# Kernel optimization log

Hardware: AMD Instinct MI355X
Metric: run time of the kernel (lower is better)

The kernel has to match this reference:

```python
import jax, jax.numpy as jnp
from jax import lax
import numpy as np

RANK, OUT_C, IN_C, K = 4, 128, 128, 3
B, H, W = 32, 56, 56


def setup_inputs() -> dict:
    key = jax.random.key(0)
    ks = jax.random.split(key, 7)
    x = jax.random.normal(ks[0], (B, IN_C, H, W), dtype=jnp.float32)
    # init_weights_normal per rank -> plain gaussian with fan-in scaling
    w = jax.random.normal(ks[1], (RANK, OUT_C, IN_C, K, K), dtype=jnp.float32) / np.sqrt(IN_C * K * K)
    cw_row = jax.random.normal(ks[2], (RANK, H, 1), dtype=jnp.float32) * 0.1
    cw_col = jax.random.normal(ks[3], (RANK, 1, W), dtype=jnp.float32) * 0.1
    b_row = jax.random.normal(ks[4], (1, 1, H, 1), dtype=jnp.float32) * 0.01
    b_col = jax.random.normal(ks[5], (1, 1, 1, W), dtype=jnp.float32) * 0.01
    b = jax.random.normal(ks[6], (1, OUT_C, 1, 1), dtype=jnp.float32) * 0.01
    return {"x": x, "w": w, "cw_row": cw_row, "cw_col": cw_col,
            "b_row": b_row, "b_col": b_col, "b": b}


def reference(x, w, cw_row, cw_col, b_row, b_col, b):
    # lrlc_nan branch: one big conv with rank*out_channels filters,
    # then per-spatial-location low-rank combining weights.
    rank, oc, ic, kh, kw = w.shape
    w_flat = w.reshape(rank * oc, ic, kh, kw)
    convs = lax.conv_general_dilated(
        x, w_flat,
        window_strides=(1, 1),
        padding=((1, 1), (1, 1)),
        dimension_numbers=("NCHW", "OIHW", "NCHW"),
    )  # [B, rank*oc, H, W]
    bsz = x.shape[0]
    hh, ww = convs.shape[2], convs.shape[3]
    convs = convs.reshape(bsz, rank, oc, hh, ww)
    # softmax over rank of per-location combining weights [rank, H, W]
    cw = jax.nn.softmax(cw_row + cw_col, axis=0)
    out = jnp.einsum("bkcxy,kxy->bcxy", convs, cw)
    # bias_pd: per-channel + per-row + per-col biases
    out = out + b + b_col + b_row
    return out
```

## Files before the change

### kernel.cpp

```cpp
#include <hip/hip_runtime.h>

#define NB 32
#define NC 128
#define NH 56
#define NW 56
#define HP 58
#define WP 58
#define KK 1152
#define NPOS 3136
#define XT_BYTES (NB * HP * WP * NC * 2)
#define AW_OFF XT_BYTES

typedef __attribute__((ext_vector_type(8))) short s16x8;
typedef __attribute__((ext_vector_type(4))) float f32x4;
typedef unsigned int u32;

__device__ __forceinline__ unsigned short f2bf(float f) {
    union { float f; unsigned int u; } v; v.f = f;
    unsigned int u = v.u + 0x7fffu + ((v.u >> 16) & 1u);
    return (unsigned short)(u >> 16);
}

__device__ __forceinline__ void gld16(const void* g, void* l) {
    __builtin_amdgcn_global_load_lds(
        (const __attribute__((address_space(1))) u32*)g,
        (__attribute__((address_space(3))) u32*)l, 16, 0, 0);
}

__global__ void k_pro(const float* __restrict__ x, const float* __restrict__ w,
                      unsigned short* __restrict__ xt, unsigned short* __restrict__ aw) {
    int blk = blockIdx.x;
    int tid = threadIdx.x;
    if (blk >= 1792) {
        int idx = (blk - 1792) * 256 + tid;
        if (idx < 512 * KK) {
            int j = idx & 7, lane = (idx >> 3) & 63, mt = (idx >> 9) & 31, s = idx >> 14;
            int m = mt * 16 + (lane & 15);
            int kg = s * 32 + (lane >> 4) * 8 + j;
            int g = kg >> 7, ic = kg & 127;
            aw[idx] = f2bf(w[(m * 128 + ic) * 9 + g]);
        }
        return;
    }
    __shared__ unsigned short tile[128 * 57];
    int b = blk / NH, y = blk % NH;
    const float* xb = x + (size_t)b * (NC * NPOS) + y * NW;
#pragma unroll
    for (int p = 0; p < 7; ++p) {
        int idx = p * 256 + tid;
        int c = idx / 14, i = idx - c * 14;
        float4 v = *(const float4*)(xb + c * NPOS + i * 4);
        unsigned short* tp = &tile[c * 57 + i * 4];
        tp[0] = f2bf(v.x); tp[1] = f2bf(v.y); tp[2] = f2bf(v.z); tp[3] = f2bf(v.w);
    }
    __syncthreads();
    unsigned short* xrow = xt + ((size_t)(b * HP + y + 1) * WP + 1) * NC;
#pragma unroll
    for (int p = 0; p < 4; ++p) {
        int idx = p * 256 + tid;
        if (idx < 896) {
            int xp = idx >> 4, cgi = idx & 15;
            s16x8 v8;
#pragma unroll
            for (int j = 0; j < 8; ++j)
                v8[j] = (short)tile[(cgi * 8 + j) * 57 + xp];
            *(s16x8*)(xrow + xp * NC + cgi * 8) = v8;
        }
    }
    if (tid < 128) {
        xt[((size_t)(b * HP + y + 1) * WP + 0) * NC + tid] = 0;
        xt[((size_t)(b * HP + y + 1) * WP + 57) * NC + tid] = 0;
    }
    if (y == 0) {
        unsigned short* r0 = xt + (size_t)(b * HP + 0) * WP * NC;
        for (int i = tid; i < WP * NC; i += 256) r0[i] = 0;
    }
    if (y == 55) {
        unsigned short* r57 = xt + (size_t)(b * HP + 57) * WP * NC;
        for (int i = tid; i < WP * NC; i += 256) r57[i] = 0;
    }
}

__global__ void __launch_bounds__(512, 2) k_main(
    const unsigned short* __restrict__ xt, const unsigned short* __restrict__ aw,
    const float* __restrict__ cwr, const float* __restrict__ cwc,
    const float* __restrict__ brow, const float* __restrict__ bcol,
    const float* __restrict__ bch, float* __restrict__ out) {
    __shared__ __align__(16) unsigned char ldsB[2][28672];

    const int tid = threadIdx.x;
    const int lane = tid & 63;
    const int wv = tid >> 6;
    const int l15 = lane & 15, quad = lane >> 4;
    const int ph = (wv & 1) * 2;
    const int blk = blockIdx.x;
    const int b = blk / 28;
    const int tile0 = (blk - b * 28) * 112;

    const unsigned char* xt_b = (const unsigned char*)xt + (size_t)b * (HP * WP * NC * 2);
    const unsigned char* gA = (const unsigned char*)aw + wv * 1024 + lane * 16;

    const unsigned char* gB[4];
    if (wv < 7) {
#pragma unroll
        for (int h = 0; h < 4; ++h) {
            int rl = h * 4 + (lane >> 4);
            int row = wv * 16 + rl;
            int pos = tile0 + row;
            int yy = pos / 56, xx = pos - yy * 56;
            int c = (lane & 15) ^ rl;
            gB[h] = xt_b + ((yy + 1) * WP + (xx + 1)) * (NC * 2) + c * 16;
        }
    }

    s16x8 Areg[2][4];
    f32x4 acc[4][7] = {};

    auto aload = [&](int s32, int pp) {
#pragma unroll
        for (int r = 0; r < 4; ++r)
            Areg[pp][r] = *(const s16x8*)(gA + s32 * 32768 + r * 8192);
    };
    auto bissue = [&](int st, int buf) {
        if (wv < 7) {
            int dy = (st * 11) >> 5, dx = st - dy * 3;
            int off = ((dy - 1) * WP + (dx - 1)) * (NC * 2);
            unsigned char* L = &ldsB[buf][wv * 4096];
#pragma unroll
            for (int h = 0; h < 4; ++h) gld16(gB[h] + off, L + h * 1024);
        }
    };

    aload(ph, 0);
    bissue(0, 0);
    __syncthreads();

    for (int st = 0; st < 9; ++st) {
        const int cur = st & 1;
        if (st < 8) bissue(st + 1, cur ^ 1);
        const unsigned char* L = &ldsB[cur][0];
#pragma unroll
        for (int j = 0; j < 4; ++j) {
            const int kkw = (j + ph) & 3;
            if (!(st == 8 && j == 3)) {
                int nslice = (j < 3) ? st * 4 + (((j + 1) + ph) & 3)
                                     : (st + 1) * 4 + ph;
                aload(nslice, (j + 1) & 1);
            }
            s16x8 bf[7];
#pragma unroll
            for (int t = 0; t < 7; ++t)
                bf[t] = *(const s16x8*)(L + (t * 16 + l15) * 256
                                          + (((kkw * 4 + quad) ^ l15) << 4));
#pragma unroll
            for (int r = 0; r < 4; ++r)
#pragma unroll
                for (int t = 0; t < 7; ++t)
                    acc[r][t] = __builtin_amdgcn_mfma_f32_16x16x32_bf16(
                        Areg[j & 1][r], bf[t], acc[r][t], 0, 0, 0);
        }
        __syncthreads();
    }

#pragma unroll
    for (int t = 0; t < 7; ++t) {
        int pos = tile0 + t * 16 + l15;
        int yy = pos / 56, xx = pos - yy * 56;
        float v0 = cwr[yy]       + cwc[xx];
        float v1 = cwr[56 + yy]  + cwc[56 + xx];
        float v2 = cwr[112 + yy] + cwc[112 + xx];
        float v3 = cwr[168 + yy] + cwc[168 + xx];
        float mx = fmaxf(fmaxf(v0, v1), fmaxf(v2, v3));
        float e0 = __expf(v0 - mx), e1 = __expf(v1 - mx);
        float e2 = __expf(v2 - mx), e3 = __expf(v3 - mx);
        float inv = 1.0f / (e0 + e1 + e2 + e3);
        float c0 = e0 * inv, c1 = e1 * inv, c2 = e2 * inv, c3 = e3 * inv;
        float rb = brow[yy] + bcol[xx];
#pragma unroll
        for (int r = 0; r < 4; ++r) {
            int ch = wv * 16 + quad * 4 + r;
            float v = acc[0][t][r] * c0 + acc[1][t][r] * c1
                    + acc[2][t][r] * c2 + acc[3][t][r] * c3;
            out[((size_t)b * NC + ch) * NPOS + pos] = v + bch[ch] + rb;
        }
    }
}

extern "C" void kernel_launch(void* const* d_in, const int* in_sizes, int n_in,
                              void* d_out, int out_size, void* d_ws, size_t ws_size,
                              hipStream_t stream) {
    const float* x    = (const float*)d_in[0];
    const float* w    = (const float*)d_in[1];
    const float* cwr  = (const float*)d_in[2];
    const float* cwc  = (const float*)d_in[3];
    const float* brow = (const float*)d_in[4];
    const float* bcol = (const float*)d_in[5];
    const float* bch  = (const float*)d_in[6];
    float* out = (float*)d_out;

    unsigned char* ws = (unsigned char*)d_ws;
    unsigned short* xt = (unsigned short*)ws;
    unsigned short* aw = (unsigned short*)(ws + AW_OFF);

    k_pro<<<4096, 256, 0, stream>>>(x, w, xt, aw);
    k_main<<<NB * 28, 512, 0, stream>>>(xt, aw, cwr, cwc, brow, bcol, bch, out);
}
```

Measured before the change: 231.0 us.

## Rewrite prologue transpose without LDS and vectorize weight packing stores

The prologue kernel now converts x to padded NHWC bf16 with one thread per (batch, row, x, 8-channel group). Each thread does strided global loads across channels and a single 16-byte store, replacing the LDS tile transpose. Weight packing now writes 8 bf16 values per thread in one vector store, and halo zeroing moves into separate blocks that use 16-byte stores. The aim is to remove the LDS round trip and the serialized per-block padding loops, at the cost of less coalesced strided loads from x.

```diff
diff --git a/kernel.cpp b/kernel.cpp
--- a/kernel.cpp
+++ b/kernel.cpp
@@ -27,57 +27,61 @@
         (__attribute__((address_space(3))) u32*)l, 16, 0, 0);
 }
 
+#define XPB 7168
+#define WPB 7456
+#define PROGRID 7912
+
 __global__ void k_pro(const float* __restrict__ x, const float* __restrict__ w,
                       unsigned short* __restrict__ xt, unsigned short* __restrict__ aw) {
     int blk = blockIdx.x;
     int tid = threadIdx.x;
-    if (blk >= 1792) {
-        int idx = (blk - 1792) * 256 + tid;
-        if (idx < 512 * KK) {
-            int j = idx & 7, lane = (idx >> 3) & 63, mt = (idx >> 9) & 31, s = idx >> 14;
-            int m = mt * 16 + (lane & 15);
-            int kg = s * 32 + (lane >> 4) * 8 + j;
-            int g = kg >> 7, ic = kg & 127;
-            aw[idx] = f2bf(w[(m * 128 + ic) * 9 + g]);
+    if (blk < XPB) {
+        int t = blk * 256 + tid;
+        int xp = t & 63;
+        int unit = t >> 6;
+        int cgi = unit & 15;
+        int by = unit >> 4;
+        int y = by % 56, b = by / 56;
+        if (xp < 56) {
+            const float* xs = x + ((size_t)(b * 128 + cgi * 8) * NPOS) + y * 56 + xp;
+            s16x8 v;
+#pragma unroll
+            for (int j = 0; j < 8; ++j)
+                v[j] = (short)f2bf(xs[(size_t)j * NPOS]);
+            *(s16x8*)(xt + (((size_t)(b * HP + y + 1) * WP) + (xp + 1)) * NC + cgi * 8) = v;
         }
         return;
     }
-    __shared__ unsigned short tile[128 * 57];
-    int b = blk / NH, y = blk % NH;
-    const float* xb = x + (size_t)b * (NC * NPOS) + y * NW;
-#pragma unroll
-    for (int p = 0; p < 7; ++p) {
-        int idx = p * 256 + tid;
-        int c = idx / 14, i = idx - c * 14;
-        float4 v = *(const float4*)(xb + c * NPOS + i * 4);
-        unsigned short* tp = &tile[c * 57 + i * 4];
-        tp[0] = f2bf(v.x); tp[1] = f2bf(v.y); tp[2] = f2bf(v.z); tp[3] = f2bf(v.w);
-    }
-    __syncthreads();
-    unsigned short* xrow = xt + ((size_t)(b * HP + y + 1) * WP + 1) * NC;
-#pragma unroll
-    for (int p = 0; p < 4; ++p) {
-        int idx = p * 256 + tid;
-        if (idx < 896) {
-            int xp = idx >> 4, cgi = idx & 15;
-            s16x8 v8;
-#pragma unroll
-            for (int j = 0; j < 8; ++j)
-                v8[j] = (short)tile[(cgi * 8 + j) * 57 + xp];
-            *(s16x8*)(xrow + xp * NC + cgi * 8) = v8;
-        }
-    }
-    if (tid < 128) {
-        xt[((size_t)(b * HP + y + 1) * WP + 0) * NC + tid] = 0;
-        xt[((size_t)(b * HP + y + 1) * WP + 57) * NC + tid] = 0;
-    }
-    if (y == 0) {
-        unsigned short* r0 = xt + (size_t)(b * HP + 0) * WP * NC;
-        for (int i = tid; i < WP * NC; i += 256) r0[i] = 0;
-    }
-    if (y == 55) {
-        unsigned short* r57 = xt + (size_t)(b * HP + 57) * WP * NC;
-        for (int i = tid; i < WP * NC; i += 256) r57[i] = 0;
+    if (blk < WPB) {
+        int t = (blk - XPB) * 256 + tid;
+        int lane = t & 63;
+        int mt = (t >> 6) & 31;
+        int s = t >> 11;
+        int m = mt * 16 + (lane & 15);
+        int kgb = s * 32 + (lane >> 4) * 8;
+        int g = kgb >> 7, icb = kgb & 127;
+        const float* ws = w + ((size_t)m * 128 + icb) * 9 + g;
+        s16x8 v;
+#pragma unroll
+        for (int j = 0; j < 8; ++j)
+            v[j] = (short)f2bf(ws[j * 9]);
+        *(s16x8*)(aw + (size_t)t * 8) = v;
+        return;
+    }
+    int h = (blk - WPB) * 256 + tid;
+    s16x8 z = {};
+    if (h < 59392) {
+        int b = h / 1856, r = h - b * 1856;
+        int row = (r < 928) ? 0 : 57;
+        int i = (r < 928) ? r : r - 928;
+        *(s16x8*)(xt + ((size_t)(b * HP + row) * WP * NC) + i * 8) = z;
+    } else {
+        int h2 = h - 59392;
+        int i = h2 & 15, rest = h2 >> 4;
+        int side = rest & 1; rest >>= 1;
+        int y = rest % 56, b = rest / 56;
+        int xcol = side ? 57 : 0;
+        *(s16x8*)(xt + (((size_t)(b * HP + y + 1) * WP) + xcol) * NC + i * 8) = z;
     }
 }
 
@@ -202,6 +206,6 @@
     unsigned short* xt = (unsigned short*)ws;
     unsigned short* aw = (unsigned short*)(ws + AW_OFF);
 
-    k_pro<<<4096, 256, 0, stream>>>(x, w, xt, aw);
+    k_pro<<<PROGRID, 256, 0, stream>>>(x, w, xt, aw);
     k_main<<<NB * 28, 512, 0, stream>>>(xt, aw, cwr, cwc, brow, bcol, bch, out);
 }
```

Measured after the change: 239.3 us. 3.6% more time.

## Prefetch a full stage of A fragments and hand-schedule barriers with waitcnt

Applied to the files above, without the earlier changes.

Replaces the per-slice A register double-buffer with a whole-stage prefetch: all 16 A fragments for the next filter tap are loaded into a second register bank while the current stage computes. The loop is manually unrolled by two so buffer indices are compile-time constants. `__syncthreads` is replaced by explicit `s_waitcnt vmcnt` counts and raw `s_barrier`s, and `s_setprio` is raised around the MFMA bursts. The goal is to hide global-load latency behind a longer compute window and avoid over-waiting at barriers. In exchange it roughly quadruples the VGPRs held for A under a 512-thread, 2-block launch bound, which risks register spills or lower occupancy.

```diff
diff --git a/kernel.cpp b/kernel.cpp
--- a/kernel.cpp
+++ b/kernel.cpp
@@ -113,13 +113,17 @@
         }
     }
 
-    s16x8 Areg[2][4];
+    s16x8 A[2][4][4];
     f32x4 acc[4][7] = {};
 
-    auto aload = [&](int s32, int pp) {
-#pragma unroll
-        for (int r = 0; r < 4; ++r)
-            Areg[pp][r] = *(const s16x8*)(gA + s32 * 32768 + r * 8192);
+    auto aloadAll = [&](int st, int bk) {
+#pragma unroll
+        for (int i = 0; i < 4; ++i) {
+            int s32 = st * 4 + ((i + ph) & 3);
+#pragma unroll
+            for (int r = 0; r < 4; ++r)
+                A[bk][i][r] = *(const s16x8*)(gA + s32 * 32768 + r * 8192);
+        }
     };
     auto bissue = [&](int st, int buf) {
         if (wv < 7) {
@@ -131,36 +135,41 @@
         }
     };
 
-    aload(ph, 0);
+#define STAGE(ST, CUR, LAST)                                                  \
+    {                                                                         \
+        if (!(LAST)) { aloadAll((ST) + 1, (CUR) ^ 1); bissue((ST) + 1, (CUR) ^ 1); } \
+        if (LAST) { asm volatile("s_waitcnt vmcnt(0)" ::: "memory"); }        \
+        else      { asm volatile("s_waitcnt vmcnt(20)" ::: "memory"); }       \
+        __builtin_amdgcn_s_barrier();                                         \
+        const unsigned char* Lb = &ldsB[CUR][0];                              \
+        _Pragma("unroll")                                                     \
+        for (int j = 0; j < 4; ++j) {                                         \
+            const int kkw = (j + ph) & 3;                                     \
+            s16x8 bf[7];                                                      \
+            _Pragma("unroll")                                                 \
+            for (int t = 0; t < 7; ++t)                                       \
+                bf[t] = *(const s16x8*)(Lb + (t * 16 + l15) * 256             \
+                                           + (((kkw * 4 + quad) ^ l15) << 4)); \
+            __builtin_amdgcn_s_setprio(1);                                    \
+            _Pragma("unroll")                                                 \
+            for (int r = 0; r < 4; ++r)                                       \
+                _Pragma("unroll")                                             \
+                for (int t = 0; t < 7; ++t)                                   \
+                    acc[r][t] = __builtin_amdgcn_mfma_f32_16x16x32_bf16(      \
+                        A[CUR][j][r], bf[t], acc[r][t], 0, 0, 0);             \
+            __builtin_amdgcn_s_setprio(0);                                    \
+        }                                                                     \
+        if (!(LAST)) __builtin_amdgcn_s_barrier();                            \
+    }
+
+    aloadAll(0, 0);
     bissue(0, 0);
-    __syncthreads();
-
-    for (int st = 0; st < 9; ++st) {
-        const int cur = st & 1;
-        if (st < 8) bissue(st + 1, cur ^ 1);
-        const unsigned char* L = &ldsB[cur][0];
-#pragma unroll
-        for (int j = 0; j < 4; ++j) {
-            const int kkw = (j + ph) & 3;
-            if (!(st == 8 && j == 3)) {
-                int nslice = (j < 3) ? st * 4 + (((j + 1) + ph) & 3)
-                                     : (st + 1) * 4 + ph;
-                aload(nslice, (j + 1) & 1);
-            }
-            s16x8 bf[7];
-#pragma unroll
-            for (int t = 0; t < 7; ++t)
-                bf[t] = *(const s16x8*)(L + (t * 16 + l15) * 256
-                                          + (((kkw * 4 + quad) ^ l15) << 4));
-#pragma unroll
-            for (int r = 0; r < 4; ++r)
-#pragma unroll
-                for (int t = 0; t < 7; ++t)
-                    acc[r][t] = __builtin_amdgcn_mfma_f32_16x16x32_bf16(
-                        Areg[j & 1][r], bf[t], acc[r][t], 0, 0, 0);
-        }
-        __syncthreads();
-    }
+    for (int st2 = 0; st2 < 4; ++st2) {
+        STAGE(st2 * 2, 0, 0)
+        STAGE(st2 * 2 + 1, 1, 0)
+    }
+    STAGE(8, 0, 1)
+#undef STAGE
 
 #pragma unroll
     for (int t = 0; t < 7; ++t) {
```

New measurement: 367.7 us. 59.2% more time.

## Stage one contiguous input slab in LDS and reuse it across all nine taps

Applied to the files above, without the earlier changes.

The main kernel used to gather a fresh 112-position input tile from global memory for each of the 9 filter taps, double-buffered with a barrier per tap. It now loads one contiguous slab of 248 padded positions into LDS once, and each tap indexes into it with a row offset, so the halo data is shared across taps. The prologue writes the transposed input with an XOR swizzle keyed on the padded position, so the raw slab copy keeps bank-conflict-free reads. This removes repeated global loads and per-tap barriers, but gives up overlap between loading and MFMA work and raises LDS use to about 62 KB per block.

```diff
diff --git a/kernel.cpp b/kernel.cpp
--- a/kernel.cpp
+++ b/kernel.cpp
@@ -64,7 +64,8 @@
 #pragma unroll
             for (int j = 0; j < 8; ++j)
                 v8[j] = (short)tile[(cgi * 8 + j) * 57 + xp];
-            *(s16x8*)(xrow + xp * NC + cgi * 8) = v8;
+            int key = ((y + 1) * WP + (xp + 1)) & 15;
+            *(s16x8*)(xrow + xp * NC + ((cgi ^ key) * 8)) = v8;
         }
     }
     if (tid < 128) {
@@ -86,7 +87,7 @@
     const float* __restrict__ cwr, const float* __restrict__ cwc,
     const float* __restrict__ brow, const float* __restrict__ bcol,
     const float* __restrict__ bch, float* __restrict__ out) {
-    __shared__ __align__(16) unsigned char ldsB[2][28672];
+    __shared__ __align__(16) unsigned char slab[248 * 256];
 
     const int tid = threadIdx.x;
     const int lane = tid & 63;
@@ -95,23 +96,29 @@
     const int ph = (wv & 1) * 2;
     const int blk = blockIdx.x;
     const int b = blk / 28;
-    const int tile0 = (blk - b * 28) * 112;
-
-    const unsigned char* xt_b = (const unsigned char*)xt + (size_t)b * (HP * WP * NC * 2);
+    const int pt = blk - b * 28;
+    const int tile0 = pt * 112;
+    const int sbase = (pt * 116) & ~15;
+
+    const unsigned char* src = (const unsigned char*)xt
+                             + ((size_t)b * (HP * WP) + sbase) * 256;
     const unsigned char* gA = (const unsigned char*)aw + wv * 1024 + lane * 16;
 
-    const unsigned char* gB[4];
-    if (wv < 7) {
-#pragma unroll
-        for (int h = 0; h < 4; ++h) {
-            int rl = h * 4 + (lane >> 4);
-            int row = wv * 16 + rl;
-            int pos = tile0 + row;
-            int yy = pos / 56, xx = pos - yy * 56;
-            int c = (lane & 15) ^ rl;
-            gB[h] = xt_b + ((yy + 1) * WP + (xx + 1)) * (NC * 2) + c * 16;
-        }
-    }
+    int R0[7];
+#pragma unroll
+    for (int t = 0; t < 7; ++t) {
+        int pos = tile0 + t * 16 + l15;
+        int yy = pos / 56, xx = pos - yy * 56;
+        R0[t] = (yy + 1) * WP + (xx + 1) - sbase;
+    }
+
+#pragma unroll
+    for (int i = 0; i < 7; ++i)
+        gld16(src + (size_t)(i * 512 + tid) * 16,
+              (unsigned char*)slab + (i * 512 + wv * 64) * 16);
+    if (wv < 6)
+        gld16(src + (size_t)(7 * 512 + tid) * 16,
+              (unsigned char*)slab + (7 * 512 + wv * 64) * 16);
 
     s16x8 Areg[2][4];
     f32x4 acc[4][7] = {};
@@ -121,24 +128,13 @@
         for (int r = 0; r < 4; ++r)
             Areg[pp][r] = *(const s16x8*)(gA + s32 * 32768 + r * 8192);
     };
-    auto bissue = [&](int st, int buf) {
-        if (wv < 7) {
-            int dy = (st * 11) >> 5, dx = st - dy * 3;
-            int off = ((dy - 1) * WP + (dx - 1)) * (NC * 2);
-            unsigned char* L = &ldsB[buf][wv * 4096];
-#pragma unroll
-            for (int h = 0; h < 4; ++h) gld16(gB[h] + off, L + h * 1024);
-        }
-    };
 
     aload(ph, 0);
-    bissue(0, 0);
     __syncthreads();
 
     for (int st = 0; st < 9; ++st) {
-        const int cur = st & 1;
-        if (st < 8) bissue(st + 1, cur ^ 1);
-        const unsigned char* L = &ldsB[cur][0];
+        int dy = (st * 11) >> 5;
+        int toff = (dy - 1) * WP + (st - dy * 3 - 1);
 #pragma unroll
         for (int j = 0; j < 4; ++j) {
             const int kkw = (j + ph) & 3;
@@ -149,9 +145,11 @@
             }
             s16x8 bf[7];
 #pragma unroll
-            for (int t = 0; t < 7; ++t)
-                bf[t] = *(const s16x8*)(L + (t * 16 + l15) * 256
-                                          + (((kkw * 4 + quad) ^ l15) << 4));
+            for (int t = 0; t < 7; ++t) {
+                int Rt = R0[t] + toff;
+                bf[t] = *(const s16x8*)((const unsigned char*)slab
+                          + (Rt << 8) + (((kkw * 4 + quad) ^ (Rt & 15)) << 4));
+            }
 #pragma unroll
             for (int r = 0; r < 4; ++r)
 #pragma unroll
@@ -159,7 +157,6 @@
                     acc[r][t] = __builtin_amdgcn_mfma_f32_16x16x32_bf16(
                         Areg[j & 1][r], bf[t], acc[r][t], 0, 0, 0);
         }
-        __syncthreads();
     }
 
 #pragma unroll
```

After: 227.7 us. About the same (-1.4%).
